# Kernel tuning notes

Measured on AMD Instinct MI355X. Metric: run time of the kernel, lower is better.

## Reference

```python
import jax, jax.numpy as jnp
import numpy as np

B, N, D = 8, 4096, 256


def setup_inputs() -> dict:
    key = jax.random.key(0)
    ks = jax.random.split(key, 4)
    seq = jax.random.normal(ks[0], (B, N, D), dtype=jnp.float32)
    W_fts = jax.random.normal(ks[1], (D, D), dtype=jnp.float32) * (1.0 / np.sqrt(D))
    w_f1 = jax.random.normal(ks[2], (D, 1), dtype=jnp.float32) * (1.0 / np.sqrt(D))
    b_f1 = jnp.zeros((1,), dtype=jnp.float32)
    w_f2 = jax.random.normal(ks[3], (D, 1), dtype=jnp.float32) * (1.0 / np.sqrt(D))
    b_f2 = jnp.zeros((1,), dtype=jnp.float32)
    bias = jnp.zeros((1,), dtype=jnp.float32)
    return {"seq": seq, "W_fts": W_fts, "w_f1": w_f1, "b_f1": b_f1,
            "w_f2": w_f2, "b_f2": b_f2, "bias": bias}


def reference(seq, W_fts, w_f1, b_f1, w_f2, b_f2, bias):
    # seq: [B, N, D]
    seq_fts = jnp.einsum('bnd,de->bne', seq, W_fts)          # values, [B, N, D]
    f_1 = seq @ w_f1 + b_f1                                   # [B, N, 1]
    f_2 = seq @ w_f2 + b_f2                                   # [B, N, 1]
    logits = f_1 + jnp.swapaxes(f_2, 1, 2)                    # broadcast add -> [B, N, N]
    coefs = jax.nn.softmax(jax.nn.leaky_relu(logits, negative_slope=0.01), axis=-1)
    vals = jnp.einsum('bnm,bmd->bnd', coefs, seq_fts)         # [B, N, D]
    ret = vals + bias
    return jax.nn.relu(ret)
```

## Files before the change

### kernel.cpp

```cpp
#include <hip/hip_runtime.h>
#include <hip/hip_bf16.h>
#include <math.h>

#define B 8
#define N 4096
#define D 256
#define BN (B*N)
#define NSUP 64
#define NS1 65
#define NR1 4097

typedef __attribute__((ext_vector_type(8))) short bf16x8;
typedef __attribute__((ext_vector_type(4))) float f32x4;

#define GLD16(src, dst) __builtin_amdgcn_global_load_lds( \
    (const __attribute__((address_space(1))) void*)(src), \
    (__attribute__((address_space(3))) void*)(dst), 16, 0, 0)

__device__ __forceinline__ ushort bf16_hi(float x) {
  __hip_bfloat16 h = __float2bfloat16(x);
  return *(ushort*)&h;
}
__device__ __forceinline__ ushort bf16_lo(float x) {
  __hip_bfloat16 h = __float2bfloat16(x);
  float hf = __bfloat162float(h);
  __hip_bfloat16 l = __float2bfloat16(x - hf);
  return *(ushort*)&l;
}

__global__ __launch_bounds__(256) void k_f1f2w(const float* __restrict__ seq,
    const float* __restrict__ w1, const float* __restrict__ b1,
    const float* __restrict__ w2, const float* __restrict__ b2,
    const float* __restrict__ W, float* __restrict__ f1, float* __restrict__ f2,
    int* __restrict__ rank, ushort* __restrict__ W3) {
  if (blockIdx.x >= BN/4) {
    int n = blockIdx.x - BN/4;
    int k = threadIdx.x;
    float x = W[(size_t)k * D + n];
    ushort hu = bf16_hi(x), lu = bf16_lo(x);
    W3[(size_t)n * 768 + k] = hu;
    W3[(size_t)n * 768 + 256 + k] = lu;
    W3[(size_t)n * 768 + 512 + k] = hu;
    return;
  }
  int wave = threadIdx.x >> 6;
  int lane = threadIdx.x & 63;
  long row = (long)blockIdx.x * 4 + wave;
  float4 v = ((const float4*)(seq + row * D))[lane];
  float4 a = ((const float4*)w1)[lane];
  float4 b = ((const float4*)w2)[lane];
  float s1 = v.x*a.x + v.y*a.y + v.z*a.z + v.w*a.w;
  float s2 = v.x*b.x + v.y*b.y + v.z*b.z + v.w*b.w;
  for (int off = 32; off; off >>= 1) {
    s1 += __shfl_xor(s1, off, 64);
    s2 += __shfl_xor(s2, off, 64);
  }
  if (lane == 0) {
    f1[row] = s1 + b1[0];
    f2[row] = s2 + b2[0];
    rank[row] = 0;
  }
}

__global__ __launch_bounds__(256) void k_rank_count(const float* __restrict__ f2,
    int* __restrict__ rank) {
  __shared__ unsigned long long skey[256];
  int b = blockIdx.z;
  int tid = threadIdx.x;
  const float* fb = f2 + (long)b * N;
  int p = blockIdx.y * 256 + tid;
  unsigned int up = __float_as_uint(fb[p]);
  up ^= (unsigned int)(((int)up >> 31) | 0x80000000);
  skey[tid] = ((unsigned long long)up << 12) | (unsigned)p;
  unsigned long long kj[4];
  int jbase = blockIdx.x * 1024;
  #pragma unroll
  for (int q = 0; q < 4; ++q) {
    int j = jbase + q * 256 + tid;
    unsigned int uj = __float_as_uint(fb[j]);
    uj ^= (unsigned int)(((int)uj >> 31) | 0x80000000);
    kj[q] = ((unsigned long long)uj << 12) | (unsigned)j;
  }
  __syncthreads();
  int c[4] = {0, 0, 0, 0};
  const ulonglong2* sk2 = (const ulonglong2*)skey;
  #pragma unroll 4
  for (int pp = 0; pp < 128; ++pp) {
    ulonglong2 kk = sk2[pp];
    #pragma unroll
    for (int q = 0; q < 4; ++q) {
      c[q] += (kk.x < kj[q]) ? 1 : 0;
      c[q] += (kk.y < kj[q]) ? 1 : 0;
    }
  }
  #pragma unroll
  for (int q = 0; q < 4; ++q)
    atomicAdd(&rank[(long)b * N + jbase + q * 256 + tid], c[q]);
}

__global__ __launch_bounds__(256) void k_scatter(const float* __restrict__ f2,
    const int* __restrict__ rank, float* __restrict__ sF2, int* __restrict__ sIdx,
    float* __restrict__ e2lo, float* __restrict__ e2hi) {
  long idx = (long)blockIdx.x * 256 + threadIdx.x;
  int b = (int)(idx >> 12);
  int j = (int)(idx & (N - 1));
  float v = f2[idx];
  int cnt = rank[idx];
  long o = (long)b * N + cnt;
  sF2[o] = v;
  sIdx[o] = j;
  e2lo[o] = expf(0.01f * v);
  e2hi[o] = expf(v);
}

__global__ __launch_bounds__(256) void k_mfma(const float* __restrict__ seq,
    const int* __restrict__ sIdx, const ushort* __restrict__ W3,
    const float* __restrict__ e2lo, const float* __restrict__ e2hi,
    float* __restrict__ Rel, float* __restrict__ Zrel,
    float* __restrict__ SupBaseLo, float* __restrict__ SupBaseHi,
    float* __restrict__ SupZlo, float* __restrict__ SupZhi) {
  __shared__ __align__(16) char smem[64 * 256 * 4];
  ushort (*As)[72] = (ushort(*)[72])smem;
  ushort (*Bs)[64] = (ushort(*)[64])(smem + 64 * 72 * 2);
  int tid = threadIdx.x;
  int wid = tid >> 6, lane = tid & 63;
  int mBase = blockIdx.x * 64;
  int b = mBase >> 12;
  int ar = tid >> 2, aq = tid & 3;
  const float* aSrc = seq + (((size_t)(b << 12)) + sIdx[mBase + ar]) * D + aq * 16;
  int lr = lane >> 3;
  int lcSw = (((lane & 7) ^ (lr & 7))) * 8;
  int wr = wid >> 1, wc = wid & 1, g = lane >> 4, r16 = lane & 15;
  int bswz = r16 & 7;

  f32x4 acc[2][8];
  #pragma unroll
  for (int m = 0; m < 2; ++m)
    #pragma unroll
    for (int n = 0; n < 8; ++n) {
      acc[m][n][0] = 0.f; acc[m][n][1] = 0.f; acc[m][n][2] = 0.f; acc[m][n][3] = 0.f;
    }

  float4 xv[4];
  #pragma unroll
  for (int i = 0; i < 4; ++i) xv[i] = *(const float4*)(aSrc + i * 4);

  for (int kt = 0; kt < 768; kt += 64) {
    ushort ou[16];
    if (kt < 512) {
      #pragma unroll
      for (int i = 0; i < 4; ++i) {
        ou[i*4+0] = bf16_hi(xv[i].x); ou[i*4+1] = bf16_hi(xv[i].y);
        ou[i*4+2] = bf16_hi(xv[i].z); ou[i*4+3] = bf16_hi(xv[i].w);
      }
    } else {
      #pragma unroll
      for (int i = 0; i < 4; ++i) {
        ou[i*4+0] = bf16_lo(xv[i].x); ou[i*4+1] = bf16_lo(xv[i].y);
        ou[i*4+2] = bf16_lo(xv[i].z); ou[i*4+3] = bf16_lo(xv[i].w);
      }
    }
    __syncthreads();
    #pragma unroll
    for (int i = 0; i < 4; ++i)
      *(ushort4*)&As[ar][aq * 16 + i * 4] =
          make_ushort4(ou[i*4+0], ou[i*4+1], ou[i*4+2], ou[i*4+3]);
    #pragma unroll
    for (int q = 0; q < 8; ++q) {
      int r0 = q * 32 + wid * 8;
      GLD16(W3 + (size_t)(r0 + lr) * 768 + kt + lcSw, &Bs[r0][0]);
    }
    if (kt < 704) {
      int nacol = (kt + 64) & 255;
      #pragma unroll
      for (int i = 0; i < 4; ++i) xv[i] = *(const float4*)(aSrc + nacol + i * 4);
    }
    __syncthreads();
    #pragma unroll
    for (int kk = 0; kk < 64; kk += 32) {
      bf16x8 av[2], bv[8];
      #pragma unroll
      for (int m = 0; m < 2; ++m)
        av[m] = *(const bf16x8*)&As[wr*32 + m*16 + r16][kk + g*8];
      int jb = (kk >> 3) + g;
      int jj = jb ^ bswz;
      #pragma unroll
      for (int n = 0; n < 8; ++n) {
        int row = wc*128 + n*16 + r16;
        bv[n] = *(const bf16x8*)((const char*)Bs + row * 128 + jj * 16);
      }
      #pragma unroll
      for (int m = 0; m < 2; ++m)
        #pragma unroll
        for (int n = 0; n < 8; ++n)
          acc[m][n] = __builtin_amdgcn_mfma_f32_16x16x32_bf16(av[m], bv[n], acc[m][n], 0, 0, 0);
    }
  }

  __syncthreads();
  float (*Vt)[256] = (float(*)[256])smem;
  int cswz = (g & 3) << 2;
  #pragma unroll
  for (int m = 0; m < 2; ++m)
    #pragma unroll
    for (int n = 0; n < 8; ++n) {
      int col = (wc*128 + n*16 + r16) ^ cswz;
      #pragma unroll
      for (int j = 0; j < 4; ++j)
        Vt[wr*32 + m*16 + g*4 + j][col] = acc[m][n][j];
    }
  __syncthreads();
  int d = tid;
  int s = (mBase >> 6) & 63;
  size_t rb = (size_t)mBase;
  float rl = 0.f, rh = 0.f;
  float* pR = Rel + ((size_t)b * NR1 + (size_t)s * 64) * 512 + d;
  #pragma unroll 8
  for (int r = 0; r < 64; ++r) {
    float wlo = e2lo[rb + r], whi = e2hi[rb + r];
    float v = Vt[r][d ^ (((r >> 2) & 3) << 2)];
    pR[(size_t)r * 512] = rl;
    pR[(size_t)r * 512 + 256] = rh;
    rl += wlo * v; rh += whi * v;
  }
  SupBaseLo[((size_t)b * NS1 + s) * D + d] = rl;
  SupBaseHi[((size_t)b * NS1 + s) * D + d] = rh;
  if (tid == 0) {
    float z = 0.f;
    #pragma unroll 8
    for (int r = 0; r < 64; ++r) { Zrel[((size_t)b * NR1 + s*64 + r) * 2] = z; z += e2lo[rb + r]; }
    SupZlo[b*NS1+s] = z;
  } else if (tid == 64) {
    float z = 0.f;
    #pragma unroll 8
    for (int r = 0; r < 64; ++r) { Zrel[((size_t)b * NR1 + s*64 + r) * 2 + 1] = z; z += e2hi[rb + r]; }
    SupZhi[b*NS1+s] = z;
  }
}

__global__ __launch_bounds__(256) void k_supscan(float* __restrict__ SupBaseLo,
    float* __restrict__ SupBaseHi, float* __restrict__ SupZlo,
    float* __restrict__ SupZhi, float* __restrict__ Rel, float* __restrict__ Zrel) {
  int b = blockIdx.x, t = threadIdx.x;
  if (t < 64) {
    float4* lo = (float4*)SupBaseLo + (size_t)b * NS1 * 64 + t;
    float4* hi = (float4*)SupBaseHi + (size_t)b * NS1 * 64 + t;
    float4 rl = {0,0,0,0}, rh = {0,0,0,0};
    for (int s = 0; s < NSUP; s += 8) {
      float4 tl[8], th[8];
      #pragma unroll
      for (int u = 0; u < 8; ++u) { tl[u] = lo[(size_t)(s+u)*64]; th[u] = hi[(size_t)(s+u)*64]; }
      #pragma unroll
      for (int u = 0; u < 8; ++u) {
        lo[(size_t)(s+u)*64] = rl; hi[(size_t)(s+u)*64] = rh;
        rl.x+=tl[u].x; rl.y+=tl[u].y; rl.z+=tl[u].z; rl.w+=tl[u].w;
        rh.x+=th[u].x; rh.y+=th[u].y; rh.z+=th[u].z; rh.w+=th[u].w;
      }
    }
    lo[(size_t)NSUP*64] = rl;
    hi[(size_t)NSUP*64] = rh;
  } else if (t < 192) {
    float4 z = {0,0,0,0};
    ((float4*)(Rel + ((size_t)b * NR1 + 4096) * 512))[t - 64] = z;
  } else if (t == 192) {
    float r = 0.f;
    for (int s = 0; s < NSUP; ++s) { float x = SupZlo[b*NS1+s]; SupZlo[b*NS1+s] = r; r += x; }
    SupZlo[b*NS1+NSUP] = r;
    Zrel[((size_t)b * NR1 + 4096) * 2] = 0.f;
  } else if (t == 193) {
    float r = 0.f;
    for (int s = 0; s < NSUP; ++s) { float x = SupZhi[b*NS1+s]; SupZhi[b*NS1+s] = r; r += x; }
    SupZhi[b*NS1+NSUP] = r;
    Zrel[((size_t)b * NR1 + 4096) * 2 + 1] = 0.f;
  }
}

__global__ __launch_bounds__(256) void k_combine2(const float* __restrict__ f1,
    const float* __restrict__ sF2, const float* __restrict__ Rel,
    const float* __restrict__ SupBaseLo, const float* __restrict__ SupBaseHi,
    const float* __restrict__ SupZlo, const float* __restrict__ SupZhi,
    const float* __restrict__ Zrel,
    const float* __restrict__ bias, float* __restrict__ out) {
  int wid = threadIdx.x >> 6, lane = threadIdx.x & 63;
  size_t i = (size_t)blockIdx.x * 4 + wid;
  int b = (int)(i >> 12);
  float f1v = f1[i];
  const float* sb = sF2 + ((size_t)b << 12);
  float t = -f1v;
  int lo = 0, hi = N;
  while (lo < hi) { int mid = (lo + hi) >> 1; if (sb[mid] <= t) lo = mid + 1; else hi = mid; }
  int k = lo;
  int s = k >> 6;
  float a = expf(f1v), cc = expf(0.01f * f1v);
  const float* rrow = Rel + ((size_t)b * NR1 + k) * 512;
  float4 rl4 = ((const float4*)rrow)[lane];
  float4 rh4 = ((const float4*)rrow)[64 + lane];
  float4 sblo = ((const float4*)SupBaseLo)[((size_t)b * NS1 + s) * 64 + lane];
  float4 sbhi = ((const float4*)SupBaseHi)[((size_t)b * NS1 + s) * 64 + lane];
  float4 pht  = ((const float4*)SupBaseHi)[((size_t)b * NS1 + NSUP) * 64 + lane];
  float2 z2 = *(const float2*)(Zrel + ((size_t)b * NR1 + k) * 2);
  float Zlo = SupZlo[b*NS1+s] + z2.x;
  float Zhi = SupZhi[b*NS1+NSUP] - SupZhi[b*NS1+s] - z2.y;
  float Z = a * Zhi + cc * Zlo;
  float rz = 1.f / Z;
  float bs = bias[0];
  float4 o4;
  o4.x = fmaxf((a*(pht.x - sbhi.x - rh4.x) + cc*(sblo.x + rl4.x)) * rz + bs, 0.f);
  o4.y = fmaxf((a*(pht.y - sbhi.y - rh4.y) + cc*(sblo.y + rl4.y)) * rz + bs, 0.f);
  o4.z = fmaxf((a*(pht.z - sbhi.z - rh4.z) + cc*(sblo.z + rl4.z)) * rz + bs, 0.f);
  o4.w = fmaxf((a*(pht.w - sbhi.w - rh4.w) + cc*(sblo.w + rl4.w)) * rz + bs, 0.f);
  ((float4*)out)[i * 64 + lane] = o4;
}

extern "C" void kernel_launch(void* const* d_in, const int* in_sizes, int n_in,
                              void* d_out, int out_size, void* d_ws, size_t ws_size,
                              hipStream_t stream) {
  const float* seq  = (const float*)d_in[0];
  const float* Wf   = (const float*)d_in[1];
  const float* w1   = (const float*)d_in[2];
  const float* b1   = (const float*)d_in[3];
  const float* w2   = (const float*)d_in[4];
  const float* b2   = (const float*)d_in[5];
  const float* bias = (const float*)d_in[6];
  float* out = (float*)d_out;

  size_t needFloats = (size_t)7*BN + (size_t)B*NR1*512 + 2*(size_t)B*NS1*D
                    + 2*(size_t)B*NS1 + 2*(size_t)B*NR1;
  size_t need = needFloats * 4 + (size_t)256 * 768 * 2;
  if (ws_size < need) return;

  float* f1   = (float*)d_ws;
  float* f2   = f1 + BN;
  float* sF2  = f2 + BN;
  float* e2lo = sF2 + BN;
  float* e2hi = e2lo + BN;
  int* sIdx   = (int*)(e2hi + BN);
  int* rank   = sIdx + BN;
  float* Rel  = (float*)(rank + BN);
  float* SupBaseLo = Rel + (size_t)B * NR1 * 512;
  float* SupBaseHi = SupBaseLo + (size_t)B * NS1 * D;
  float* SupZlo = SupBaseHi + (size_t)B * NS1 * D;
  float* SupZhi = SupZlo + B * NS1;
  float* Zrel   = SupZhi + B * NS1;
  ushort* W3 = (ushort*)(Zrel + 2 * (size_t)B * NR1);

  k_f1f2w<<<dim3(BN/4 + 256), 256, 0, stream>>>(seq, w1, b1, w2, b2, Wf,
      f1, f2, rank, W3);
  k_rank_count<<<dim3(N/1024, N/256, B), 256, 0, stream>>>(f2, rank);
  k_scatter<<<dim3(BN/256), 256, 0, stream>>>(f2, rank, sF2, sIdx, e2lo, e2hi);
  k_mfma<<<dim3(BN/64), 256, 0, stream>>>(seq, sIdx, W3, e2lo, e2hi,
      Rel, Zrel, SupBaseLo, SupBaseHi, SupZlo, SupZhi);
  k_supscan<<<dim3(B), 256, 0, stream>>>(SupBaseLo, SupBaseHi, SupZlo, SupZhi,
      Rel, Zrel);
  k_combine2<<<dim3(BN/4), 256, 0, stream>>>(f1, sF2, Rel,
      SupBaseLo, SupBaseHi, SupZlo, SupZhi, Zrel, bias, out);
}
```

Baseline: 88.64 us.

## Replace per-row prefix table with bucketed query walk over stored values

The MFMA kernel no longer writes a full per-row prefix-sum table (Rel/Zrel). It now writes the projected values Vs and per-superblock weighted sums, using in-register reductions. A new bucketing kernel binary-searches each query's split point and appends it to a per-(batch, superblock) list. A walk kernel then scans the 64 value rows of each superblock, emitting outputs for the queries whose split falls on each row, which removes the supscan and combine kernels and the large prefix table traffic. Buckets are capped at 256 entries, so skewed inputs could silently drop outputs, and the walk is serial per block with scattered output writes.

```diff
diff --git a/kernel.cpp b/kernel.cpp
--- a/kernel.cpp
+++ b/kernel.cpp
@@ -7,8 +7,7 @@
 #define D 256
 #define BN (B*N)
 #define NSUP 64
-#define NS1 65
-#define NR1 4097
+#define CAP 256
 
 typedef __attribute__((ext_vector_type(8))) short bf16x8;
 typedef __attribute__((ext_vector_type(4))) float f32x4;
@@ -32,9 +31,14 @@
     const float* __restrict__ w1, const float* __restrict__ b1,
     const float* __restrict__ w2, const float* __restrict__ b2,
     const float* __restrict__ W, float* __restrict__ f1, float* __restrict__ f2,
-    int* __restrict__ rank, ushort* __restrict__ W3) {
+    int* __restrict__ rank, int* __restrict__ bcnt, ushort* __restrict__ W3) {
   if (blockIdx.x >= BN/4) {
-    int n = blockIdx.x - BN/4;
+    int xb = blockIdx.x - BN/4;
+    if (xb == 256) {
+      if (threadIdx.x < 256) { bcnt[threadIdx.x] = 0; bcnt[256 + threadIdx.x] = 0; }
+      return;
+    }
+    int n = xb;
     int k = threadIdx.x;
     float x = W[(size_t)k * D + n];
     ushort hu = bf16_hi(x), lu = bf16_lo(x);
@@ -113,13 +117,30 @@
   e2hi[o] = expf(v);
 }
 
+__global__ __launch_bounds__(256) void k_bucket(const float* __restrict__ f1,
+    const float* __restrict__ sF2, int* __restrict__ bcnt,
+    unsigned* __restrict__ blist) {
+  int i = blockIdx.x * 256 + threadIdx.x;
+  int b = i >> 12, il = i & 4095;
+  float t = -f1[i];
+  const float* sb = sF2 + ((size_t)b << 12);
+  int lo = 0, hi = N;
+  while (lo < hi) { int mid = (lo + hi) >> 1; if (sb[mid] <= t) lo = mid + 1; else hi = mid; }
+  int k = lo;
+  int s = k >> 6; if (s > 63) s = 63;
+  int pos = atomicAdd(&bcnt[b * 64 + s], 1);
+  if (pos < CAP) blist[(size_t)(b * 64 + s) * CAP + pos] = ((unsigned)k << 12) | (unsigned)il;
+}
+
 __global__ __launch_bounds__(256) void k_mfma(const float* __restrict__ seq,
     const int* __restrict__ sIdx, const ushort* __restrict__ W3,
     const float* __restrict__ e2lo, const float* __restrict__ e2hi,
-    float* __restrict__ Rel, float* __restrict__ Zrel,
-    float* __restrict__ SupBaseLo, float* __restrict__ SupBaseHi,
-    float* __restrict__ SupZlo, float* __restrict__ SupZhi) {
-  __shared__ __align__(16) char smem[64 * 256 * 4];
+    float* __restrict__ Vs, float* __restrict__ SupBaseLo,
+    float* __restrict__ SupBaseHi, float* __restrict__ SupZlo,
+    float* __restrict__ SupZhi) {
+  __shared__ __align__(16) char smem[64*72*2 + 256*64*2];
+  __shared__ float partLo[2][256], partHi[2][256];
+  __shared__ float wlS[64], whS[64];
   ushort (*As)[72] = (ushort(*)[72])smem;
   ushort (*Bs)[64] = (ushort(*)[64])(smem + 64 * 72 * 2);
   int tid = threadIdx.x;
@@ -197,119 +218,164 @@
     }
   }
 
-  __syncthreads();
-  float (*Vt)[256] = (float(*)[256])smem;
-  int cswz = (g & 3) << 2;
+  size_t rb = (size_t)mBase;
+  int s = (mBase >> 6) & 63;
+  if (tid < 64) { wlS[tid] = e2lo[rb + tid]; whS[tid] = e2hi[rb + tid]; }
   #pragma unroll
   for (int m = 0; m < 2; ++m)
     #pragma unroll
     for (int n = 0; n < 8; ++n) {
-      int col = (wc*128 + n*16 + r16) ^ cswz;
-      #pragma unroll
-      for (int j = 0; j < 4; ++j)
-        Vt[wr*32 + m*16 + g*4 + j][col] = acc[m][n][j];
-    }
-  __syncthreads();
-  int d = tid;
-  int s = (mBase >> 6) & 63;
-  size_t rb = (size_t)mBase;
-  float rl = 0.f, rh = 0.f;
-  float* pR = Rel + ((size_t)b * NR1 + (size_t)s * 64) * 512 + d;
+      int col = wc*128 + n*16 + r16;
+      #pragma unroll
+      for (int j = 0; j < 4; ++j) {
+        int row = mBase + wr*32 + m*16 + g*4 + j;
+        Vs[(size_t)row * D + col] = acc[m][n][j];
+      }
+    }
+  __syncthreads();
+  float plo[8], phi[8];
+  #pragma unroll
+  for (int n = 0; n < 8; ++n) { plo[n] = 0.f; phi[n] = 0.f; }
+  #pragma unroll
+  for (int m = 0; m < 2; ++m)
+    #pragma unroll
+    for (int j = 0; j < 4; ++j) {
+      int lr2 = wr*32 + m*16 + g*4 + j;
+      float wL = wlS[lr2], wH = whS[lr2];
+      #pragma unroll
+      for (int n = 0; n < 8; ++n) {
+        plo[n] += wL * acc[m][n][j];
+        phi[n] += wH * acc[m][n][j];
+      }
+    }
+  #pragma unroll
+  for (int n = 0; n < 8; ++n) {
+    plo[n] += __shfl_xor(plo[n], 16, 64); plo[n] += __shfl_xor(plo[n], 32, 64);
+    phi[n] += __shfl_xor(phi[n], 16, 64); phi[n] += __shfl_xor(phi[n], 32, 64);
+  }
+  if (g == 0) {
+    #pragma unroll
+    for (int n = 0; n < 8; ++n) {
+      partLo[wr][wc*128 + n*16 + r16] = plo[n];
+      partHi[wr][wc*128 + n*16 + r16] = phi[n];
+    }
+  }
+  __syncthreads();
+  SupBaseLo[((size_t)b * 64 + s) * D + tid] = partLo[0][tid] + partLo[1][tid];
+  SupBaseHi[((size_t)b * 64 + s) * D + tid] = partHi[0][tid] + partHi[1][tid];
+  if (tid < 64) {
+    float z = wlS[tid];
+    for (int off = 1; off < 64; off <<= 1) z += __shfl_xor(z, off, 64);
+    if (tid == 0) SupZlo[b * 64 + s] = z;
+  } else if (tid < 128) {
+    float z = whS[tid - 64];
+    for (int off = 1; off < 64; off <<= 1) z += __shfl_xor(z, off, 64);
+    if (tid == 64) SupZhi[b * 64 + s] = z;
+  }
+}
+
+__global__ __launch_bounds__(256) void k_walk(const float* __restrict__ f1,
+    const float* __restrict__ e2lo, const float* __restrict__ e2hi,
+    const float* __restrict__ Vs, const float* __restrict__ SupBaseLo,
+    const float* __restrict__ SupBaseHi, const float* __restrict__ SupZlo,
+    const float* __restrict__ SupZhi, const int* __restrict__ bcnt,
+    const unsigned* __restrict__ blist, const float* __restrict__ bias,
+    float* __restrict__ out) {
+  int s = blockIdx.x & 63, b = blockIdx.x >> 6;
+  int cnt = bcnt[b * 64 + s];
+  if (cnt == 0) return;
+  if (cnt > CAP) cnt = CAP;
+  int tid = threadIdx.x;
+  __shared__ float f1a[CAP], f1c[CAP];
+  __shared__ unsigned sorted_[CAP];
+  __shared__ int binStart[66];
+  __shared__ int binOff[65];
+  __shared__ float wl[64], wh[64];
+
+  float baseLo = 0.f, baseHi = 0.f, totHi = 0.f;
+  float zbLo = 0.f, zbHi = 0.f, ztHi = 0.f;
+  const float* sbl = SupBaseLo + (size_t)b * 64 * D + tid;
+  const float* sbh = SupBaseHi + (size_t)b * 64 * D + tid;
   #pragma unroll 8
-  for (int r = 0; r < 64; ++r) {
-    float wlo = e2lo[rb + r], whi = e2hi[rb + r];
-    float v = Vt[r][d ^ (((r >> 2) & 3) << 2)];
-    pR[(size_t)r * 512] = rl;
-    pR[(size_t)r * 512 + 256] = rh;
-    rl += wlo * v; rh += whi * v;
-  }
-  SupBaseLo[((size_t)b * NS1 + s) * D + d] = rl;
-  SupBaseHi[((size_t)b * NS1 + s) * D + d] = rh;
-  if (tid == 0) {
-    float z = 0.f;
-    #pragma unroll 8
-    for (int r = 0; r < 64; ++r) { Zrel[((size_t)b * NR1 + s*64 + r) * 2] = z; z += e2lo[rb + r]; }
-    SupZlo[b*NS1+s] = z;
-  } else if (tid == 64) {
-    float z = 0.f;
-    #pragma unroll 8
-    for (int r = 0; r < 64; ++r) { Zrel[((size_t)b * NR1 + s*64 + r) * 2 + 1] = z; z += e2hi[rb + r]; }
-    SupZhi[b*NS1+s] = z;
-  }
-}
-
-__global__ __launch_bounds__(256) void k_supscan(float* __restrict__ SupBaseLo,
-    float* __restrict__ SupBaseHi, float* __restrict__ SupZlo,
-    float* __restrict__ SupZhi, float* __restrict__ Rel, float* __restrict__ Zrel) {
-  int b = blockIdx.x, t = threadIdx.x;
-  if (t < 64) {
-    float4* lo = (float4*)SupBaseLo + (size_t)b * NS1 * 64 + t;
-    float4* hi = (float4*)SupBaseHi + (size_t)b * NS1 * 64 + t;
-    float4 rl = {0,0,0,0}, rh = {0,0,0,0};
-    for (int s = 0; s < NSUP; s += 8) {
-      float4 tl[8], th[8];
-      #pragma unroll
-      for (int u = 0; u < 8; ++u) { tl[u] = lo[(size_t)(s+u)*64]; th[u] = hi[(size_t)(s+u)*64]; }
-      #pragma unroll
-      for (int u = 0; u < 8; ++u) {
-        lo[(size_t)(s+u)*64] = rl; hi[(size_t)(s+u)*64] = rh;
-        rl.x+=tl[u].x; rl.y+=tl[u].y; rl.z+=tl[u].z; rl.w+=tl[u].w;
-        rh.x+=th[u].x; rh.y+=th[u].y; rh.z+=th[u].z; rh.w+=th[u].w;
-      }
-    }
-    lo[(size_t)NSUP*64] = rl;
-    hi[(size_t)NSUP*64] = rh;
-  } else if (t < 192) {
-    float4 z = {0,0,0,0};
-    ((float4*)(Rel + ((size_t)b * NR1 + 4096) * 512))[t - 64] = z;
-  } else if (t == 192) {
-    float r = 0.f;
-    for (int s = 0; s < NSUP; ++s) { float x = SupZlo[b*NS1+s]; SupZlo[b*NS1+s] = r; r += x; }
-    SupZlo[b*NS1+NSUP] = r;
-    Zrel[((size_t)b * NR1 + 4096) * 2] = 0.f;
-  } else if (t == 193) {
-    float r = 0.f;
-    for (int s = 0; s < NSUP; ++s) { float x = SupZhi[b*NS1+s]; SupZhi[b*NS1+s] = r; r += x; }
-    SupZhi[b*NS1+NSUP] = r;
-    Zrel[((size_t)b * NR1 + 4096) * 2 + 1] = 0.f;
-  }
-}
-
-__global__ __launch_bounds__(256) void k_combine2(const float* __restrict__ f1,
-    const float* __restrict__ sF2, const float* __restrict__ Rel,
-    const float* __restrict__ SupBaseLo, const float* __restrict__ SupBaseHi,
-    const float* __restrict__ SupZlo, const float* __restrict__ SupZhi,
-    const float* __restrict__ Zrel,
-    const float* __restrict__ bias, float* __restrict__ out) {
-  int wid = threadIdx.x >> 6, lane = threadIdx.x & 63;
-  size_t i = (size_t)blockIdx.x * 4 + wid;
-  int b = (int)(i >> 12);
-  float f1v = f1[i];
-  const float* sb = sF2 + ((size_t)b << 12);
-  float t = -f1v;
-  int lo = 0, hi = N;
-  while (lo < hi) { int mid = (lo + hi) >> 1; if (sb[mid] <= t) lo = mid + 1; else hi = mid; }
-  int k = lo;
-  int s = k >> 6;
-  float a = expf(f1v), cc = expf(0.01f * f1v);
-  const float* rrow = Rel + ((size_t)b * NR1 + k) * 512;
-  float4 rl4 = ((const float4*)rrow)[lane];
-  float4 rh4 = ((const float4*)rrow)[64 + lane];
-  float4 sblo = ((const float4*)SupBaseLo)[((size_t)b * NS1 + s) * 64 + lane];
-  float4 sbhi = ((const float4*)SupBaseHi)[((size_t)b * NS1 + s) * 64 + lane];
-  float4 pht  = ((const float4*)SupBaseHi)[((size_t)b * NS1 + NSUP) * 64 + lane];
-  float2 z2 = *(const float2*)(Zrel + ((size_t)b * NR1 + k) * 2);
-  float Zlo = SupZlo[b*NS1+s] + z2.x;
-  float Zhi = SupZhi[b*NS1+NSUP] - SupZhi[b*NS1+s] - z2.y;
-  float Z = a * Zhi + cc * Zlo;
-  float rz = 1.f / Z;
-  float bs = bias[0];
-  float4 o4;
-  o4.x = fmaxf((a*(pht.x - sbhi.x - rh4.x) + cc*(sblo.x + rl4.x)) * rz + bs, 0.f);
-  o4.y = fmaxf((a*(pht.y - sbhi.y - rh4.y) + cc*(sblo.y + rl4.y)) * rz + bs, 0.f);
-  o4.z = fmaxf((a*(pht.z - sbhi.z - rh4.z) + cc*(sblo.z + rl4.z)) * rz + bs, 0.f);
-  o4.w = fmaxf((a*(pht.w - sbhi.w - rh4.w) + cc*(sblo.w + rl4.w)) * rz + bs, 0.f);
-  ((float4*)out)[i * 64 + lane] = o4;
+  for (int sp = 0; sp < 64; ++sp) {
+    float l = sbl[(size_t)sp * D];
+    float h = sbh[(size_t)sp * D];
+    float zl = SupZlo[b * 64 + sp], zh = SupZhi[b * 64 + sp];
+    if (sp < s) { baseLo += l; baseHi += h; zbLo += zl; zbHi += zh; }
+    totHi += h; ztHi += zh;
+  }
+
+  size_t rb = ((size_t)b << 12) + (size_t)s * 64;
+  if (tid < 64) { wl[tid] = e2lo[rb + tid]; wh[tid] = e2hi[rb + tid]; }
+  if (tid < 65) binOff[tid] = 0;
+  __syncthreads();
+  unsigned pk = 0; int myr = -1;
+  if (tid < cnt) {
+    pk = blist[(size_t)(b * 64 + s) * CAP + tid];
+    myr = (int)(pk >> 12) - s * 64;
+    atomicAdd(&binOff[myr], 1);
+  }
+  __syncthreads();
+  if (tid < 64) {
+    int v = binOff[tid];
+    int x = v;
+    #pragma unroll
+    for (int off = 1; off < 64; off <<= 1) {
+      int y = __shfl_up(x, off, 64);
+      if (tid >= off) x += y;
+    }
+    binStart[tid] = x - v;
+    if (tid == 63) { binStart[64] = x; binStart[65] = x + binOff[64]; }
+  }
+  __syncthreads();
+  if (tid < 65) binOff[tid] = 0;
+  __syncthreads();
+  if (tid < cnt) {
+    int pos = binStart[myr] + atomicAdd(&binOff[myr], 1);
+    sorted_[pos] = pk;
+  }
+  __syncthreads();
+  if (tid < cnt) {
+    unsigned q = sorted_[tid];
+    int io = q & 4095;
+    float f = f1[((size_t)b << 12) + io];
+    f1a[tid] = expf(f);
+    f1c[tid] = expf(0.01f * f);
+  }
+  __syncthreads();
+
+  float Slo = baseLo, Shi = baseHi;
+  float zlo = zbLo, zhi = zbHi;
+  const float* vrow = Vs + rb * D + tid;
+  float bsc = bias[0];
+  for (int r16b = 0; r16b < 64; r16b += 16) {
+    float vv[16];
+    #pragma unroll
+    for (int u = 0; u < 16; ++u) vv[u] = vrow[(size_t)(r16b + u) * D];
+    #pragma unroll
+    for (int u = 0; u < 16; ++u) {
+      int r = r16b + u;
+      for (int e = binStart[r]; e < binStart[r + 1]; ++e) {
+        unsigned q = sorted_[e];
+        int io = q & 4095;
+        float a = f1a[e], c2 = f1c[e];
+        float Z = a * (ztHi - zhi) + c2 * zlo;
+        float o = (a * (totHi - Shi) + c2 * Slo) / Z + bsc;
+        out[((((size_t)b << 12) + io) << 8) + tid] = fmaxf(o, 0.f);
+      }
+      float wL = wl[r], wH = wh[r];
+      Slo += wL * vv[u]; Shi += wH * vv[u];
+      zlo += wL; zhi += wH;
+    }
+  }
+  for (int e = binStart[64]; e < binStart[65]; ++e) {
+    unsigned q = sorted_[e];
+    int io = q & 4095;
+    float a = f1a[e], c2 = f1c[e];
+    float Z = a * (ztHi - zhi) + c2 * zlo;
+    float o = (a * (totHi - Shi) + c2 * Slo) / Z + bsc;
+    out[((((size_t)b << 12) + io) << 8) + tid] = fmaxf(o, 0.f);
+  }
 }
 
 extern "C" void kernel_launch(void* const* d_in, const int* in_sizes, int n_in,
@@ -324,8 +390,8 @@
   const float* bias = (const float*)d_in[6];
   float* out = (float*)d_out;
 
-  size_t needFloats = (size_t)7*BN + (size_t)B*NR1*512 + 2*(size_t)B*NS1*D
-                    + 2*(size_t)B*NS1 + 2*(size_t)B*NR1;
+  size_t needFloats = (size_t)7*BN + (size_t)BN*D + 2*(size_t)B*NSUP*D
+                    + 2*(size_t)B*NSUP + (size_t)B*NSUP + (size_t)B*NSUP*CAP;
   size_t need = needFloats * 4 + (size_t)256 * 768 * 2;
   if (ws_size < need) return;
 
@@ -336,22 +402,22 @@
   float* e2hi = e2lo + BN;
   int* sIdx   = (int*)(e2hi + BN);
   int* rank   = sIdx + BN;
-  float* Rel  = (float*)(rank + BN);
-  float* SupBaseLo = Rel + (size_t)B * NR1 * 512;
-  float* SupBaseHi = SupBaseLo + (size_t)B * NS1 * D;
-  float* SupZlo = SupBaseHi + (size_t)B * NS1 * D;
-  float* SupZhi = SupZlo + B * NS1;
-  float* Zrel   = SupZhi + B * NS1;
-  ushort* W3 = (ushort*)(Zrel + 2 * (size_t)B * NR1);
-
-  k_f1f2w<<<dim3(BN/4 + 256), 256, 0, stream>>>(seq, w1, b1, w2, b2, Wf,
-      f1, f2, rank, W3);
+  float* Vs   = (float*)(rank + BN);
+  float* SupBaseLo = Vs + (size_t)BN * D;
+  float* SupBaseHi = SupBaseLo + (size_t)B * NSUP * D;
+  float* SupZlo = SupBaseHi + (size_t)B * NSUP * D;
+  float* SupZhi = SupZlo + B * NSUP;
+  int* bcnt     = (int*)(SupZhi + B * NSUP);
+  unsigned* blist = (unsigned*)(bcnt + B * NSUP);
+  ushort* W3 = (ushort*)(blist + (size_t)B * NSUP * CAP);
+
+  k_f1f2w<<<dim3(BN/4 + 257), 256, 0, stream>>>(seq, w1, b1, w2, b2, Wf,
+      f1, f2, rank, bcnt, W3);
   k_rank_count<<<dim3(N/1024, N/256, B), 256, 0, stream>>>(f2, rank);
   k_scatter<<<dim3(BN/256), 256, 0, stream>>>(f2, rank, sF2, sIdx, e2lo, e2hi);
+  k_bucket<<<dim3(BN/256), 256, 0, stream>>>(f1, sF2, bcnt, blist);
   k_mfma<<<dim3(BN/64), 256, 0, stream>>>(seq, sIdx, W3, e2lo, e2hi,
-      Rel, Zrel, SupBaseLo, SupBaseHi, SupZlo, SupZhi);
-  k_supscan<<<dim3(B), 256, 0, stream>>>(SupBaseLo, SupBaseHi, SupZlo, SupZhi,
-      Rel, Zrel);
-  k_combine2<<<dim3(BN/4), 256, 0, stream>>>(f1, sF2, Rel,
-      SupBaseLo, SupBaseHi, SupZlo, SupZhi, Zrel, bias, out);
-}
+      Vs, SupBaseLo, SupBaseHi, SupZlo, SupZhi);
+  k_walk<<<dim3(B * NSUP), 256, 0, stream>>>(f1, e2lo, e2hi, Vs,
+      SupBaseLo, SupBaseHi, SupZlo, SupZhi, bcnt, blist, bias, out);
+}
```

New measurement: 101.3 us. 1.14x slower.

## Stage full bf16 A row tile in LDS once instead of per-k-step conversion

Applied to the files above, without the earlier changes.

The k_mfma kernel now loads and converts the entire 64x256 gathered seq tile to bf16-hi in shared memory up front, and rewrites it with bf16-lo values only once, at the hi-to-lo switch. The old version reloaded and reconverted a 64-column slice each k step. This removes the repeated per-iteration global loads and conversions of A and reorders the W3 prefetch to follow the compute. In exchange it uses more LDS, which may lower occupancy, and the W3 load still sits between two barriers without double buffering.

```diff
diff --git a/kernel.cpp b/kernel.cpp
--- a/kernel.cpp
+++ b/kernel.cpp
@@ -9,6 +9,7 @@
 #define NSUP 64
 #define NS1 65
 #define NR1 4097
+#define ALD 264
 
 typedef __attribute__((ext_vector_type(8))) short bf16x8;
 typedef __attribute__((ext_vector_type(4))) float f32x4;
@@ -119,15 +120,15 @@
     float* __restrict__ Rel, float* __restrict__ Zrel,
     float* __restrict__ SupBaseLo, float* __restrict__ SupBaseHi,
     float* __restrict__ SupZlo, float* __restrict__ SupZhi) {
-  __shared__ __align__(16) char smem[64 * 256 * 4];
-  ushort (*As)[72] = (ushort(*)[72])smem;
-  ushort (*Bs)[64] = (ushort(*)[64])(smem + 64 * 72 * 2);
+  __shared__ __align__(16) char smem[64*ALD*2 + 256*64*2];
+  ushort (*As)[ALD] = (ushort(*)[ALD])smem;
+  ushort (*Bs)[64] = (ushort(*)[64])(smem + 64 * ALD * 2);
   int tid = threadIdx.x;
   int wid = tid >> 6, lane = tid & 63;
   int mBase = blockIdx.x * 64;
   int b = mBase >> 12;
   int ar = tid >> 2, aq = tid & 3;
-  const float* aSrc = seq + (((size_t)(b << 12)) + sIdx[mBase + ar]) * D + aq * 16;
+  const float* aRow = seq + (((size_t)(b << 12)) + sIdx[mBase + ar]) * D;
   int lr = lane >> 3;
   int lcSw = (((lane & 7) ^ (lr & 7))) * 8;
   int wr = wid >> 1, wc = wid & 1, g = lane >> 4, r16 = lane & 15;
@@ -141,47 +142,32 @@
       acc[m][n][0] = 0.f; acc[m][n][1] = 0.f; acc[m][n][2] = 0.f; acc[m][n][3] = 0.f;
     }
 
-  float4 xv[4];
-  #pragma unroll
-  for (int i = 0; i < 4; ++i) xv[i] = *(const float4*)(aSrc + i * 4);
+  #pragma unroll
+  for (int q = 0; q < 8; ++q) {
+    int r0 = q * 32 + wid * 8;
+    GLD16(W3 + (size_t)(r0 + lr) * 768 + 0 + lcSw, &Bs[r0][0]);
+  }
+  #pragma unroll
+  for (int c = 0; c < 4; ++c) {
+    float4 x[4];
+    #pragma unroll
+    for (int i = 0; i < 4; ++i)
+      x[i] = *(const float4*)(aRow + aq * 64 + c * 16 + i * 4);
+    #pragma unroll
+    for (int i = 0; i < 4; ++i)
+      *(ushort4*)&As[ar][aq * 64 + c * 16 + i * 4] = make_ushort4(
+          bf16_hi(x[i].x), bf16_hi(x[i].y), bf16_hi(x[i].z), bf16_hi(x[i].w));
+  }
+  __syncthreads();
 
   for (int kt = 0; kt < 768; kt += 64) {
-    ushort ou[16];
-    if (kt < 512) {
-      #pragma unroll
-      for (int i = 0; i < 4; ++i) {
-        ou[i*4+0] = bf16_hi(xv[i].x); ou[i*4+1] = bf16_hi(xv[i].y);
-        ou[i*4+2] = bf16_hi(xv[i].z); ou[i*4+3] = bf16_hi(xv[i].w);
-      }
-    } else {
-      #pragma unroll
-      for (int i = 0; i < 4; ++i) {
-        ou[i*4+0] = bf16_lo(xv[i].x); ou[i*4+1] = bf16_lo(xv[i].y);
-        ou[i*4+2] = bf16_lo(xv[i].z); ou[i*4+3] = bf16_lo(xv[i].w);
-      }
-    }
-    __syncthreads();
-    #pragma unroll
-    for (int i = 0; i < 4; ++i)
-      *(ushort4*)&As[ar][aq * 16 + i * 4] =
-          make_ushort4(ou[i*4+0], ou[i*4+1], ou[i*4+2], ou[i*4+3]);
-    #pragma unroll
-    for (int q = 0; q < 8; ++q) {
-      int r0 = q * 32 + wid * 8;
-      GLD16(W3 + (size_t)(r0 + lr) * 768 + kt + lcSw, &Bs[r0][0]);
-    }
-    if (kt < 704) {
-      int nacol = (kt + 64) & 255;
-      #pragma unroll
-      for (int i = 0; i < 4; ++i) xv[i] = *(const float4*)(aSrc + nacol + i * 4);
-    }
-    __syncthreads();
+    int acol = kt & 255;
     #pragma unroll
     for (int kk = 0; kk < 64; kk += 32) {
       bf16x8 av[2], bv[8];
       #pragma unroll
       for (int m = 0; m < 2; ++m)
-        av[m] = *(const bf16x8*)&As[wr*32 + m*16 + r16][kk + g*8];
+        av[m] = *(const bf16x8*)&As[wr*32 + m*16 + r16][acol + kk + g*8];
       int jb = (kk >> 3) + g;
       int jj = jb ^ bswz;
       #pragma unroll
@@ -195,9 +181,31 @@
         for (int n = 0; n < 8; ++n)
           acc[m][n] = __builtin_amdgcn_mfma_f32_16x16x32_bf16(av[m], bv[n], acc[m][n], 0, 0, 0);
     }
-  }
-
-  __syncthreads();
+    __syncthreads();
+    if (kt == 448) {
+      #pragma unroll
+      for (int c = 0; c < 4; ++c) {
+        float4 x[4];
+        #pragma unroll
+        for (int i = 0; i < 4; ++i)
+          x[i] = *(const float4*)(aRow + aq * 64 + c * 16 + i * 4);
+        #pragma unroll
+        for (int i = 0; i < 4; ++i)
+          *(ushort4*)&As[ar][aq * 64 + c * 16 + i * 4] = make_ushort4(
+              bf16_lo(x[i].x), bf16_lo(x[i].y), bf16_lo(x[i].z), bf16_lo(x[i].w));
+      }
+    }
+    if (kt < 704) {
+      int nkt = kt + 64;
+      #pragma unroll
+      for (int q = 0; q < 8; ++q) {
+        int r0 = q * 32 + wid * 8;
+        GLD16(W3 + (size_t)(r0 + lr) * 768 + nkt + lcSw, &Bs[r0][0]);
+      }
+    }
+    __syncthreads();
+  }
+
   float (*Vt)[256] = (float(*)[256])smem;
   int cswz = (g & 3) << 2;
   #pragma unroll
```

Measured after the change: 101.9 us. +14.9%, slower.
